# Kernel optimization log

Measured on AMD Instinct MI355X. Metric: run time of the kernel, lower is better.

The kernel has to match this reference:

```python
import jax, jax.numpy as jnp
import numpy as np

N_NODES = 100000
N_EDGES = 1600000
IN_C, HID_C, OUT_C = 128, 128, 64


def setup_inputs() -> dict:
    key = jax.random.key(0)
    k = jax.random.split(key, 5)
    x = jax.random.normal(k[0], (N_NODES, IN_C), dtype=jnp.float32)
    edge_index = jax.random.randint(k[1], (2, N_EDGES), 0, N_NODES, dtype=jnp.int32)
    # Glorot-ish scaling for the GCNConv linear weights
    W1 = jax.random.normal(k[2], (IN_C, HID_C), dtype=jnp.float32) * (1.0 / np.sqrt(IN_C))
    b1 = jnp.zeros((HID_C,), dtype=jnp.float32)
    W2 = jax.random.normal(k[3], (HID_C, OUT_C), dtype=jnp.float32) * (1.0 / np.sqrt(HID_C))
    b2 = jnp.zeros((OUT_C,), dtype=jnp.float32)
    return {"x": x, "edge_index": edge_index, "W1": W1, "b1": b1, "W2": W2, "b2": b2}


def _gcn_conv(h, W, b, src, dst, deg_inv_sqrt, n):
    # h: [N, F_in] -> linear transform, then deg-normalized scatter-add over edges
    h = h @ W  # [N, F_out]
    norm = deg_inv_sqrt[src] * deg_inv_sqrt[dst]  # [E+N] (self-loops included)
    msgs = h[src] * norm[:, None]  # gather + scale
    out = jax.ops.segment_sum(msgs, dst, num_segments=n)  # scatter-add to dst
    return out + b


def reference(x, edge_index, W1, b1, W2, b2):
    n = x.shape[0]
    loops = jnp.arange(n, dtype=edge_index.dtype)
    src = jnp.concatenate([edge_index[0], loops])  # add self-loops (PyG default)
    dst = jnp.concatenate([edge_index[1], loops])
    deg = jax.ops.segment_sum(jnp.ones_like(dst, dtype=x.dtype), dst, num_segments=n)
    deg_inv_sqrt = jax.lax.rsqrt(deg)  # deg >= 1 due to self-loops

    h = _gcn_conv(x, W1, b1, src, dst, deg_inv_sqrt, n)
    h = jax.nn.relu(h)
    # F.dropout(training=False) is identity at inference
    h = _gcn_conv(h, W2, b2, src, dst, deg_inv_sqrt, n)
    return jax.nn.log_softmax(h, axis=1)
```

## Files before the change

### kernel.cpp

```cpp
#include <hip/hip_runtime.h>
#include <hip/hip_bf16.h>


typedef unsigned short ushortT;
typedef unsigned char ucharT;
typedef __attribute__((ext_vector_type(8))) short short8v;
typedef __attribute__((ext_vector_type(4))) float float4v;
typedef __attribute__((ext_vector_type(2))) float float2v;
typedef __attribute__((ext_vector_type(8))) unsigned short ushort8v;

__device__ __forceinline__ float bf2f(ushortT u) {
  union { unsigned int i; float f; } x;
  x.i = ((unsigned int)u) << 16;
  return x.f;
}

__device__ __forceinline__ ushortT f2bf(float f) {
  __hip_bfloat16 h = __float2bfloat16(f);
  return *(ushortT*)&h;
}

__device__ __forceinline__ ucharT f2fp8(float f) {
  unsigned int w = __builtin_amdgcn_cvt_pk_fp8_f32(f, f, 0, false);
  return (ucharT)(w & 0xff);
}

__device__ __forceinline__ void fp8x8_to_f32(unsigned int lo, unsigned int hi,
                                             float* f) {
  float2v p0 = __builtin_amdgcn_cvt_pk_f32_fp8(lo, false);
  float2v p1 = __builtin_amdgcn_cvt_pk_f32_fp8(lo, true);
  float2v p2 = __builtin_amdgcn_cvt_pk_f32_fp8(hi, false);
  float2v p3 = __builtin_amdgcn_cvt_pk_f32_fp8(hi, true);
  f[0] = p0[0]; f[1] = p0[1]; f[2] = p1[0]; f[3] = p1[1];
  f[4] = p2[0]; f[5] = p2[1]; f[6] = p3[0]; f[7] = p3[1];
}

__device__ __forceinline__ void fp8x4_to_f32(unsigned int w, float* f) {
  float2v p0 = __builtin_amdgcn_cvt_pk_f32_fp8(w, false);
  float2v p1 = __builtin_amdgcn_cvt_pk_f32_fp8(w, true);
  f[0] = p0[0]; f[1] = p0[1]; f[2] = p1[0]; f[3] = p1[1];
}

__global__ void probe_k(const ushortT* __restrict__ xr, int* __restrict__ flag) {
  const int lane = threadIdx.x;
  float v = bf2f(xr[lane]);
  bool sane = isfinite(v) && fabsf(v) < 1e4f;
  unsigned long long m = __ballot(sane);
  if (lane == 0) flag[0] = (m == ~0ull) ? 1 : 0;
}

__global__ __launch_bounds__(256) void wprep_k(const void* __restrict__ W1v,
                                               const void* __restrict__ W2v,
                                               const int* __restrict__ flag,
                                               ushortT* __restrict__ Wt1,
                                               ushortT* __restrict__ Wt2) {
  const int i = blockIdx.x * 256 + threadIdx.x;
  const bool isbf = (flag[0] != 0);
  if (i < 16384) {
    int nn = i & 127, k = i >> 7;
    ushortT v = isbf ? ((const ushortT*)W1v)[k * 128 + nn]
                     : f2bf(((const float*)W1v)[k * 128 + nn]);
    Wt1[nn * 128 + k] = v;
  } else if (i < 24576) {
    int j = i - 16384;
    int nn = j & 63, k = j >> 6;
    ushortT v = isbf ? ((const ushortT*)W2v)[k * 64 + nn]
                     : f2bf(((const float*)W2v)[k * 64 + nn]);
    Wt2[nn * 128 + k] = v;
  }
}


__global__ __launch_bounds__(256) void bhist_k(const int* __restrict__ dst, int E, int B,
                                               int* __restrict__ gbc) {
  __shared__ int h[512];
  const int tid = threadIdx.x;
  for (int i = tid; i < B; i += 256) h[i] = 0;
  __syncthreads();
  const int i0 = blockIdx.x * 8192;
  const int iend = min(i0 + 8192, E);
  for (int i = i0 + tid; i < iend; i += 256) atomicAdd(&h[dst[i] >> 8], 1);
  __syncthreads();
  for (int i = tid; i < B; i += 256)
    if (h[i]) atomicAdd(&gbc[i], h[i]);
}

__global__ __launch_bounds__(256) void bscan_k(const int* __restrict__ gbc, int B,
                                               int* __restrict__ bbase,
                                               int* __restrict__ gcur) {
  __shared__ int p[256];
  const int t = threadIdx.x;
  int a = (2 * t < B) ? gbc[2 * t] : 0;
  int b = (2 * t + 1 < B) ? gbc[2 * t + 1] : 0;
  const int sum = a + b;
  p[t] = sum;
  __syncthreads();
  int run = sum;
  for (int off = 1; off < 256; off <<= 1) {
    int v = (t >= off) ? p[t - off] : 0;
    __syncthreads();
    run += v;
    p[t] = run;
    __syncthreads();
  }
  const int excl = run - sum;
  if (2 * t < B) { bbase[2 * t] = excl; gcur[2 * t] = excl; }
  if (2 * t + 1 < B) { bbase[2 * t + 1] = excl + a; gcur[2 * t + 1] = excl + a; }
}

__global__ __launch_bounds__(256) void bin_k(const int* __restrict__ srcv,
                                             const int* __restrict__ dstv, int E, int B,
                                             int* __restrict__ gcur,
                                             int* __restrict__ tmp) {
  __shared__ int hist[512];
  __shared__ int base[512];
  const int tid = threadIdx.x;
  const int i0 = blockIdx.x * 8192;
  const int iend = min(i0 + 8192, E);
  for (int i = tid; i < B; i += 256) hist[i] = 0;
  __syncthreads();
  for (int i = i0 + tid; i < iend; i += 256) atomicAdd(&hist[dstv[i] >> 8], 1);
  __syncthreads();
  for (int i = tid; i < B; i += 256) {
    int h = hist[i];
    base[i] = h ? atomicAdd(&gcur[i], h) : 0;
    hist[i] = 0;
  }
  __syncthreads();
  for (int i = i0 + tid; i < iend; i += 256) {
    int d = dstv[i];
    int s = srcv[i];
    int b = d >> 8;
    int l = atomicAdd(&hist[b], 1);
    tmp[base[b] + l] = s | ((d & 255) << 17);
  }
}

__global__ __launch_bounds__(256) void csr_k(const int* __restrict__ tmp,
                                             const int* __restrict__ bbase,
                                             const int* __restrict__ gbc, int n,
                                             int* __restrict__ row_ptr,
                                             int* __restrict__ cnt,
                                             float* __restrict__ dis,
                                             int* __restrict__ col) {
  __shared__ int lhist[256];
  __shared__ int lexcl[256];
  const int b = blockIdx.x;
  const int tid = threadIdx.x;
  const int e0 = bbase[b];
  const int e1 = e0 + gbc[b];
  lhist[tid] = 0;
  __syncthreads();
  for (int i = e0 + tid; i < e1; i += 256) atomicAdd(&lhist[tmp[i] >> 17], 1);
  __syncthreads();
  const int v = lhist[tid];
  int run = v;
  lexcl[tid] = run;
  __syncthreads();
  for (int off = 1; off < 256; off <<= 1) {
    int t = (tid >= off) ? lexcl[tid - off] : 0;
    __syncthreads();
    run += t;
    lexcl[tid] = run;
    __syncthreads();
  }
  const int excl = run - v;
  const int node = (b << 8) + tid;
  if (node < n) {
    row_ptr[node] = e0 + excl;
    cnt[node] = v;
    dis[node] = rsqrtf((float)(v + 1));
  }
  lhist[tid] = 0;
  lexcl[tid] = excl;
  __syncthreads();
  for (int i = e0 + tid; i < e1; i += 256) {
    int p = tmp[i];
    int dloc = p >> 17;
    int s = p & 131071;
    int l = atomicAdd(&lhist[dloc], 1);
    col[e0 + lexcl[dloc] + l] = s;
  }
}

__global__ __launch_bounds__(256) void gemm1_k(const void* __restrict__ xv,
                                               const ushortT* __restrict__ Wt1,
                                               const float* __restrict__ dis,
                                               const int* __restrict__ flag,
                                               ucharT* __restrict__ Hb8, int n) {
  __shared__ ushortT sA[64 * 132];
  __shared__ ushortT sW[128 * 132];
  const bool isbf = (flag[0] != 0);
  const int tid = threadIdx.x;
  const int rb = blockIdx.x * 64;
  const int wave = tid >> 6;
  const int lane = tid & 63;
  const int m = lane & 15;
  const int quad = lane >> 4;

  if (isbf) {
    for (int i = tid; i < 2048; i += 256) {
      int r = i >> 5, c4 = (i & 31) * 4;
      ushort4 u = make_ushort4(0, 0, 0, 0);
      if (rb + r < n) u = *(const ushort4*)((const ushortT*)xv + (size_t)(rb + r) * 128 + c4);
      *(ushort4*)&sA[r * 132 + c4] = u;
    }
  } else {
    for (int i = tid; i < 2048; i += 256) {
      int r = i >> 5, c4 = (i & 31) * 4;
      float4 v = make_float4(0.f, 0.f, 0.f, 0.f);
      if (rb + r < n) v = *(const float4*)((const float*)xv + (size_t)(rb + r) * 128 + c4);
      ushort4 u;
      u.x = f2bf(v.x); u.y = f2bf(v.y); u.z = f2bf(v.z); u.w = f2bf(v.w);
      *(ushort4*)&sA[r * 132 + c4] = u;
    }
  }
  for (int i = tid; i < 4096; i += 256) {
    int nn = i >> 5, k4 = (i & 31) * 4;
    *(ushort4*)&sW[nn * 132 + k4] = *(const ushort4*)&Wt1[nn * 128 + k4];
  }
  __syncthreads();

  float4v acc[8];
#pragma unroll
  for (int t = 0; t < 8; ++t) acc[t] = (float4v)(0.f);

  const int arow = wave * 16 + m;
#pragma unroll
  for (int kc = 0; kc < 4; ++kc) {
    short8v af = *(const short8v*)&sA[arow * 132 + kc * 32 + quad * 8];
#pragma unroll
    for (int nb = 0; nb < 8; ++nb) {
      short8v bf = *(const short8v*)&sW[(nb * 16 + m) * 132 + kc * 32 + quad * 8];
      acc[nb] = __builtin_amdgcn_mfma_f32_16x16x32_bf16(af, bf, acc[nb], 0, 0, 0);
    }
  }

#pragma unroll
  for (int r = 0; r < 4; ++r) {
    int grow = rb + wave * 16 + quad * 4 + r;
    if (grow <= n) {
      float sc = (grow < n) ? dis[grow] : 0.f;
#pragma unroll
      for (int nb = 0; nb < 8; ++nb)
        Hb8[(size_t)grow * 128 + nb * 16 + m] =
            (grow < n) ? f2fp8(sc * acc[nb][r]) : (ucharT)0;
    }
  }
}

__global__ __launch_bounds__(256) void agg1_k(const ucharT* __restrict__ Hb8,
                                              const int* __restrict__ col,
                                              const int* __restrict__ row_ptr,
                                              const int* __restrict__ count,
                                              const float* __restrict__ dis,
                                              const void* __restrict__ b1v,
                                              const int* __restrict__ flag,
                                              ushortT* __restrict__ Ab, int n) {
  const int node = blockIdx.x * 4 + (threadIdx.x >> 6);
  if (node >= n) return;
  const bool isbf = (flag[0] != 0);
  const int lane = threadIdx.x & 63;
  const int quad = lane >> 4;
  const int c8 = (lane & 15) * 8;
  const int start = __builtin_amdgcn_readfirstlane(row_ptr[node]);
  const int cnt = __builtin_amdgcn_readfirstlane(count[node]);

  float2v acc[4];
#pragma unroll
  for (int k = 0; k < 4; ++k) acc[k] = (float2v)(0.f);

  for (int e0 = 0; e0 < cnt; e0 += 16) {
#pragma unroll
    for (int g = 0; g < 4; ++g) {
      const int e = e0 + g * 4 + quad;
      int s = col[start + e];
      s = (e < cnt) ? s : n;
      uint2 h = *(const uint2*)&Hb8[((unsigned)s << 7) + (unsigned)c8];
      acc[0] += __builtin_amdgcn_cvt_pk_f32_fp8(h.x, false);
      acc[1] += __builtin_amdgcn_cvt_pk_f32_fp8(h.x, true);
      acc[2] += __builtin_amdgcn_cvt_pk_f32_fp8(h.y, false);
      acc[3] += __builtin_amdgcn_cvt_pk_f32_fp8(h.y, true);
    }
  }

  float accs[8];
#pragma unroll
  for (int k = 0; k < 4; ++k) { accs[2 * k] = acc[k][0]; accs[2 * k + 1] = acc[k][1]; }
#pragma unroll
  for (int k = 0; k < 8; ++k) {
    accs[k] += __shfl_xor(accs[k], 16);
    accs[k] += __shfl_xor(accs[k], 32);
  }

  const float din = dis[node];
  uint2 hsp = *(const uint2*)&Hb8[((unsigned)node << 7) + (unsigned)c8];
  float hs[8];
  fp8x8_to_f32(hsp.x, hsp.y, hs);
  float b[8];
  if (isbf) {
    ushort8v bb = *(const ushort8v*)((const ushortT*)b1v + c8);
#pragma unroll
    for (int k = 0; k < 8; ++k) b[k] = bf2f(bb[k]);
  } else {
    const float* bf = (const float*)b1v + c8;
#pragma unroll
    for (int k = 0; k < 8; ++k) b[k] = bf[k];
  }
  if (quad == 0) {
    ushort8v o;
#pragma unroll
    for (int k = 0; k < 8; ++k)
      o[k] = f2bf(fmaxf(fmaf(din, accs[k] + hs[k], b[k]), 0.f));
    *(ushort8v*)&Ab[(size_t)node * 128 + c8] = o;
  }
}

__global__ __launch_bounds__(256) void gemm2_k(const ushortT* __restrict__ Ab,
                                               const ushortT* __restrict__ Wt2,
                                               const float* __restrict__ dis,
                                               ucharT* __restrict__ H2b8, int n) {
  __shared__ ushortT sA[64 * 132];
  __shared__ ushortT sW[64 * 132];
  const int tid = threadIdx.x;
  const int rb = blockIdx.x * 64;
  const int wave = tid >> 6;
  const int lane = tid & 63;
  const int m = lane & 15;
  const int quad = lane >> 4;

  for (int i = tid; i < 2048; i += 256) {
    int r = i >> 5, c4 = (i & 31) * 4;
    ushort4 u = make_ushort4(0, 0, 0, 0);
    if (rb + r < n) u = *(const ushort4*)&Ab[(size_t)(rb + r) * 128 + c4];
    *(ushort4*)&sA[r * 132 + c4] = u;
  }
  for (int i = tid; i < 2048; i += 256) {
    int nn = i >> 5, k4 = (i & 31) * 4;
    *(ushort4*)&sW[nn * 132 + k4] = *(const ushort4*)&Wt2[nn * 128 + k4];
  }
  __syncthreads();

  float4v acc[4];
#pragma unroll
  for (int t = 0; t < 4; ++t) acc[t] = (float4v)(0.f);

  const int arow = wave * 16 + m;
#pragma unroll
  for (int kc = 0; kc < 4; ++kc) {
    short8v af = *(const short8v*)&sA[arow * 132 + kc * 32 + quad * 8];
#pragma unroll
    for (int nb = 0; nb < 4; ++nb) {
      short8v bf = *(const short8v*)&sW[(nb * 16 + m) * 132 + kc * 32 + quad * 8];
      acc[nb] = __builtin_amdgcn_mfma_f32_16x16x32_bf16(af, bf, acc[nb], 0, 0, 0);
    }
  }

#pragma unroll
  for (int r = 0; r < 4; ++r) {
    int grow = rb + wave * 16 + quad * 4 + r;
    if (grow <= n) {
      float sc = (grow < n) ? dis[grow] : 0.f;
#pragma unroll
      for (int nb = 0; nb < 4; ++nb)
        H2b8[(size_t)grow * 64 + nb * 16 + m] =
            (grow < n) ? f2fp8(sc * acc[nb][r]) : (ucharT)0;
    }
  }
}

__global__ __launch_bounds__(256) void agg2_k(const ucharT* __restrict__ H2b8,
                                              const int* __restrict__ col,
                                              const int* __restrict__ row_ptr,
                                              const int* __restrict__ count,
                                              const float* __restrict__ dis,
                                              const void* __restrict__ b2v,
                                              const int* __restrict__ flag,
                                              void* __restrict__ outv, int n) {
  const int node = blockIdx.x * 4 + (threadIdx.x >> 6);
  if (node >= n) return;
  const bool isbf = (flag[0] != 0);
  const int lane = threadIdx.x & 63;
  const int quad = lane >> 4;
  const int c4 = (lane & 15) * 4;
  const int start = __builtin_amdgcn_readfirstlane(row_ptr[node]);
  const int cnt = __builtin_amdgcn_readfirstlane(count[node]);

  float2v acc[2];
  acc[0] = (float2v)(0.f);
  acc[1] = (float2v)(0.f);

  for (int e0 = 0; e0 < cnt; e0 += 16) {
#pragma unroll
    for (int g = 0; g < 4; ++g) {
      const int e = e0 + g * 4 + quad;
      int s = col[start + e];
      s = (e < cnt) ? s : n;
      unsigned int h = *(const unsigned int*)&H2b8[((unsigned)s << 6) + (unsigned)c4];
      acc[0] += __builtin_amdgcn_cvt_pk_f32_fp8(h, false);
      acc[1] += __builtin_amdgcn_cvt_pk_f32_fp8(h, true);
    }
  }

  float av[4] = {acc[0][0], acc[0][1], acc[1][0], acc[1][1]};
#pragma unroll
  for (int k = 0; k < 4; ++k) {
    av[k] += __shfl_xor(av[k], 16);
    av[k] += __shfl_xor(av[k], 32);
  }

  const float din = dis[node];
  unsigned int hsp = *(const unsigned int*)&H2b8[((unsigned)node << 6) + (unsigned)c4];
  float hs[4];
  fp8x4_to_f32(hsp, hs);
  float b[4];
  if (isbf) {
    ushort4 bb = *(const ushort4*)((const ushortT*)b2v + c4);
    b[0] = bf2f(bb.x); b[1] = bf2f(bb.y); b[2] = bf2f(bb.z); b[3] = bf2f(bb.w);
  } else {
    const float* bf = (const float*)b2v + c4;
#pragma unroll
    for (int k = 0; k < 4; ++k) b[k] = bf[k];
  }
  float v[4];
#pragma unroll
  for (int k = 0; k < 4; ++k) v[k] = fmaf(din, av[k] + hs[k], b[k]);

  float mx = fmaxf(fmaxf(v[0], v[1]), fmaxf(v[2], v[3]));
  for (int off = 1; off < 16; off <<= 1) mx = fmaxf(mx, __shfl_xor(mx, off));
  float ssum = __expf(v[0] - mx) + __expf(v[1] - mx) + __expf(v[2] - mx) + __expf(v[3] - mx);
  for (int off = 1; off < 16; off <<= 1) ssum += __shfl_xor(ssum, off);
  const float lse = mx + __logf(ssum);

  if (quad == 0) {
    if (isbf) {
      ushort4 o;
      o.x = f2bf(v[0] - lse); o.y = f2bf(v[1] - lse);
      o.z = f2bf(v[2] - lse); o.w = f2bf(v[3] - lse);
      *(ushort4*)((__hip_bfloat16*)outv + (size_t)node * 64 + c4) = o;
    } else {
      float4 o = make_float4(v[0] - lse, v[1] - lse, v[2] - lse, v[3] - lse);
      *(float4*)((float*)outv + (size_t)node * 64 + c4) = o;
    }
  }
}


extern "C" void kernel_launch(void* const* d_in, const int* in_sizes, int n_in,
                              void* d_out, int out_size, void* d_ws, size_t ws_size,
                              hipStream_t stream) {
  const void* x  = d_in[0];
  const int*  ei = (const int*)d_in[1];
  const void* W1 = d_in[2];
  const void* b1 = d_in[3];
  const void* W2 = d_in[4];
  const void* b2 = d_in[5];

  const int n = in_sizes[0] / 128;
  const int E = in_sizes[1] / 2;
  const int B = (n + 255) >> 8;
  const int* srcv = ei;
  const int* dstv = ei + E;

  char* p = (char*)d_ws;
  auto alloc = [&](size_t bytes) {
    char* q = p;
    p += (bytes + 255) & ~(size_t)255;
    return q;
  };
  ucharT* Hb8 = (ucharT*)alloc((size_t)(n + 1) * 128);
  ucharT* H2b8 = (ucharT*)alloc((size_t)(n + 1) * 64);
  ushortT* Ab = (ushortT*)alloc((size_t)n * 128 * 2);
  float* dis = (float*)alloc((size_t)n * 4);
  int* cntA = (int*)alloc((size_t)n * 4);
  int* row_ptr = (int*)alloc((size_t)n * 4);
  int* gbc = (int*)alloc(512 * 4);
  int* bbase = (int*)alloc(512 * 4);
  int* gcur = (int*)alloc(512 * 4);
  int* flag = (int*)alloc(64 * 4);
  ushortT* Wt1 = (ushortT*)alloc(16384 * 2);
  ushortT* Wt2 = (ushortT*)alloc(8192 * 2);
  int* tmp = (int*)alloc((size_t)E * 4);
  int* col = (int*)alloc(((size_t)E + 64) * 4);

  (void)hipMemsetAsync(gbc, 0, 512 * sizeof(int), stream);

  const int gChunks = (E + 8191) / 8192;

  probe_k<<<1, 64, 0, stream>>>((const ushortT*)x, flag);
  wprep_k<<<96, 256, 0, stream>>>(W1, W2, flag, Wt1, Wt2);
  bhist_k<<<gChunks, 256, 0, stream>>>(dstv, E, B, gbc);
  bscan_k<<<1, 256, 0, stream>>>(gbc, B, bbase, gcur);
  bin_k<<<gChunks, 256, 0, stream>>>(srcv, dstv, E, B, gcur, tmp);
  csr_k<<<B, 256, 0, stream>>>(tmp, bbase, gbc, n, row_ptr, cntA, dis, col);

  gemm1_k<<<(n + 63) / 64, 256, 0, stream>>>(x, Wt1, dis, flag, Hb8, n);
  agg1_k<<<(n + 3) / 4, 256, 0, stream>>>(Hb8, col, row_ptr, cntA, dis, b1, flag, Ab, n);
  gemm2_k<<<(n + 63) / 64, 256, 0, stream>>>(Ab, Wt2, dis, H2b8, n);
  agg2_k<<<(n + 3) / 4, 256, 0, stream>>>(H2b8, col, row_ptr, cntA, dis, b2, flag, d_out, n);
}
```

Before: 282.6 us.

## Map four nodes per wave in aggregation, pack row_ptr/count, inline dtype probe

The aggregation kernels now give each 16-lane quarter-wave its own destination node instead of spreading one node's edges across the whole wave. This removes the cross-quad shuffle reduction and the idle lanes on low-degree nodes, but the loop runs to the maximum degree among the four nodes, so lanes diverge when degrees differ. Row pointer and count are packed into one int2 so each node needs a single load. The separate probe kernel is dropped and every kernel recomputes the dtype check with a ballot, which saves one launch. The col buffer padding is enlarged to cover the longer over-reads.

Result: faster. 256.8 us (-9.1%).

```diff
diff --git a/kernel.cpp b/kernel.cpp
--- a/kernel.cpp
+++ b/kernel.cpp
@@ -41,21 +41,21 @@
   f[0] = p0[0]; f[1] = p0[1]; f[2] = p1[0]; f[3] = p1[1];
 }
 
-__global__ void probe_k(const ushortT* __restrict__ xr, int* __restrict__ flag) {
-  const int lane = threadIdx.x;
+__device__ __forceinline__ bool probe_isbf(const void* xv) {
+  const ushortT* xr = (const ushortT*)xv;
+  const int lane = threadIdx.x & 63;
   float v = bf2f(xr[lane]);
   bool sane = isfinite(v) && fabsf(v) < 1e4f;
-  unsigned long long m = __ballot(sane);
-  if (lane == 0) flag[0] = (m == ~0ull) ? 1 : 0;
+  return __ballot(sane) == ~0ull;
 }
 
 __global__ __launch_bounds__(256) void wprep_k(const void* __restrict__ W1v,
                                                const void* __restrict__ W2v,
-                                               const int* __restrict__ flag,
+                                               const void* __restrict__ xv,
                                                ushortT* __restrict__ Wt1,
                                                ushortT* __restrict__ Wt2) {
+  const bool isbf = probe_isbf(xv);
   const int i = blockIdx.x * 256 + threadIdx.x;
-  const bool isbf = (flag[0] != 0);
   if (i < 16384) {
     int nn = i & 127, k = i >> 7;
     ushortT v = isbf ? ((const ushortT*)W1v)[k * 128 + nn]
@@ -139,8 +139,7 @@
 __global__ __launch_bounds__(256) void csr_k(const int* __restrict__ tmp,
                                              const int* __restrict__ bbase,
                                              const int* __restrict__ gbc, int n,
-                                             int* __restrict__ row_ptr,
-                                             int* __restrict__ cnt,
+                                             int2* __restrict__ rpc,
                                              float* __restrict__ dis,
                                              int* __restrict__ col) {
   __shared__ int lhist[256];
@@ -167,8 +166,7 @@
   const int excl = run - v;
   const int node = (b << 8) + tid;
   if (node < n) {
-    row_ptr[node] = e0 + excl;
-    cnt[node] = v;
+    rpc[node] = make_int2(e0 + excl, v);
     dis[node] = rsqrtf((float)(v + 1));
   }
   lhist[tid] = 0;
@@ -186,11 +184,10 @@
 __global__ __launch_bounds__(256) void gemm1_k(const void* __restrict__ xv,
                                                const ushortT* __restrict__ Wt1,
                                                const float* __restrict__ dis,
-                                               const int* __restrict__ flag,
                                                ucharT* __restrict__ Hb8, int n) {
   __shared__ ushortT sA[64 * 132];
   __shared__ ushortT sW[128 * 132];
-  const bool isbf = (flag[0] != 0);
+  const bool isbf = probe_isbf(xv);
   const int tid = threadIdx.x;
   const int rb = blockIdx.x * 64;
   const int wave = tid >> 6;
@@ -251,32 +248,55 @@
 
 __global__ __launch_bounds__(256) void agg1_k(const ucharT* __restrict__ Hb8,
                                               const int* __restrict__ col,
-                                              const int* __restrict__ row_ptr,
-                                              const int* __restrict__ count,
+                                              const int2* __restrict__ rpc,
                                               const float* __restrict__ dis,
                                               const void* __restrict__ b1v,
-                                              const int* __restrict__ flag,
+                                              const void* __restrict__ xv,
                                               ushortT* __restrict__ Ab, int n) {
-  const int node = blockIdx.x * 4 + (threadIdx.x >> 6);
-  if (node >= n) return;
-  const bool isbf = (flag[0] != 0);
-  const int lane = threadIdx.x & 63;
+  const bool isbf = probe_isbf(xv);
+  const int tid = threadIdx.x;
+  const int lane = tid & 63;
+  const int wave = tid >> 6;
   const int quad = lane >> 4;
-  const int c8 = (lane & 15) * 8;
-  const int start = __builtin_amdgcn_readfirstlane(row_ptr[node]);
-  const int cnt = __builtin_amdgcn_readfirstlane(count[node]);
+  const int m = lane & 15;
+  const int c8 = m * 8;
+  const int node = blockIdx.x * 16 + wave * 4 + quad;
+  const bool valid = node < n;
+  const int nd = valid ? node : (n - 1);
+
+  const int2 rc = rpc[nd];
+  const int start = rc.x;
+  const int cnt = valid ? rc.y : 0;
+  const float din = dis[nd];
+
+  const uint2 hsp = *(const uint2*)&Hb8[((unsigned)(valid ? node : n) << 7) + (unsigned)c8];
+  float b[8];
+  if (isbf) {
+    ushort8v bb = *(const ushort8v*)((const ushortT*)b1v + c8);
+#pragma unroll
+    for (int k = 0; k < 8; ++k) b[k] = bf2f(bb[k]);
+  } else {
+    const float* bf = (const float*)b1v + c8;
+#pragma unroll
+    for (int k = 0; k < 8; ++k) b[k] = bf[k];
+  }
+
+  int cmax = cnt;
+  cmax = max(cmax, __shfl_xor(cmax, 16));
+  cmax = max(cmax, __shfl_xor(cmax, 32));
+  const int cmaxs = __builtin_amdgcn_readfirstlane(cmax);
 
   float2v acc[4];
 #pragma unroll
   for (int k = 0; k < 4; ++k) acc[k] = (float2v)(0.f);
 
-  for (int e0 = 0; e0 < cnt; e0 += 16) {
-#pragma unroll
-    for (int g = 0; g < 4; ++g) {
-      const int e = e0 + g * 4 + quad;
-      int s = col[start + e];
-      s = (e < cnt) ? s : n;
-      uint2 h = *(const uint2*)&Hb8[((unsigned)s << 7) + (unsigned)c8];
+  for (int e = 0; e < cmaxs; e += 4) {
+#pragma unroll
+    for (int u = 0; u < 4; ++u) {
+      const int ee = e + u;
+      int s = col[start + ee];
+      s = (ee < cnt) ? s : n;
+      const uint2 h = *(const uint2*)&Hb8[((unsigned)s << 7) + (unsigned)c8];
       acc[0] += __builtin_amdgcn_cvt_pk_f32_fp8(h.x, false);
       acc[1] += __builtin_amdgcn_cvt_pk_f32_fp8(h.x, true);
       acc[2] += __builtin_amdgcn_cvt_pk_f32_fp8(h.y, false);
@@ -284,34 +304,15 @@
     }
   }
 
-  float accs[8];
-#pragma unroll
-  for (int k = 0; k < 4; ++k) { accs[2 * k] = acc[k][0]; accs[2 * k + 1] = acc[k][1]; }
-#pragma unroll
-  for (int k = 0; k < 8; ++k) {
-    accs[k] += __shfl_xor(accs[k], 16);
-    accs[k] += __shfl_xor(accs[k], 32);
-  }
-
-  const float din = dis[node];
-  uint2 hsp = *(const uint2*)&Hb8[((unsigned)node << 7) + (unsigned)c8];
-  float hs[8];
-  fp8x8_to_f32(hsp.x, hsp.y, hs);
-  float b[8];
-  if (isbf) {
-    ushort8v bb = *(const ushort8v*)((const ushortT*)b1v + c8);
-#pragma unroll
-    for (int k = 0; k < 8; ++k) b[k] = bf2f(bb[k]);
-  } else {
-    const float* bf = (const float*)b1v + c8;
-#pragma unroll
-    for (int k = 0; k < 8; ++k) b[k] = bf[k];
-  }
-  if (quad == 0) {
+  if (valid) {
+    float hs[8];
+    fp8x8_to_f32(hsp.x, hsp.y, hs);
     ushort8v o;
 #pragma unroll
-    for (int k = 0; k < 8; ++k)
-      o[k] = f2bf(fmaxf(fmaf(din, accs[k] + hs[k], b[k]), 0.f));
+    for (int k = 0; k < 4; ++k) {
+      o[2 * k]     = f2bf(fmaxf(fmaf(din, acc[k][0] + hs[2 * k],     b[2 * k]),     0.f));
+      o[2 * k + 1] = f2bf(fmaxf(fmaf(din, acc[k][1] + hs[2 * k + 1], b[2 * k + 1]), 0.f));
+    }
     *(ushort8v*)&Ab[(size_t)node * 128 + c8] = o;
   }
 }
@@ -371,48 +372,29 @@
 
 __global__ __launch_bounds__(256) void agg2_k(const ucharT* __restrict__ H2b8,
                                               const int* __restrict__ col,
-                                              const int* __restrict__ row_ptr,
-                                              const int* __restrict__ count,
+                                              const int2* __restrict__ rpc,
                                               const float* __restrict__ dis,
                                               const void* __restrict__ b2v,
-                                              const int* __restrict__ flag,
+                                              const void* __restrict__ xv,
                                               void* __restrict__ outv, int n) {
-  const int node = blockIdx.x * 4 + (threadIdx.x >> 6);
-  if (node >= n) return;
-  const bool isbf = (flag[0] != 0);
-  const int lane = threadIdx.x & 63;
+  const bool isbf = probe_isbf(xv);
+  const int tid = threadIdx.x;
+  const int lane = tid & 63;
+  const int wave = tid >> 6;
   const int quad = lane >> 4;
-  const int c4 = (lane & 15) * 4;
-  const int start = __builtin_amdgcn_readfirstlane(row_ptr[node]);
-  const int cnt = __builtin_amdgcn_readfirstlane(count[node]);
-
-  float2v acc[2];
-  acc[0] = (float2v)(0.f);
-  acc[1] = (float2v)(0.f);
-
-  for (int e0 = 0; e0 < cnt; e0 += 16) {
-#pragma unroll
-    for (int g = 0; g < 4; ++g) {
-      const int e = e0 + g * 4 + quad;
-      int s = col[start + e];
-      s = (e < cnt) ? s : n;
-      unsigned int h = *(const unsigned int*)&H2b8[((unsigned)s << 6) + (unsigned)c4];
-      acc[0] += __builtin_amdgcn_cvt_pk_f32_fp8(h, false);
-      acc[1] += __builtin_amdgcn_cvt_pk_f32_fp8(h, true);
-    }
-  }
-
-  float av[4] = {acc[0][0], acc[0][1], acc[1][0], acc[1][1]};
-#pragma unroll
-  for (int k = 0; k < 4; ++k) {
-    av[k] += __shfl_xor(av[k], 16);
-    av[k] += __shfl_xor(av[k], 32);
-  }
-
-  const float din = dis[node];
-  unsigned int hsp = *(const unsigned int*)&H2b8[((unsigned)node << 6) + (unsigned)c4];
-  float hs[4];
-  fp8x4_to_f32(hsp, hs);
+  const int m = lane & 15;
+  const int c4 = m * 4;
+  const int node = blockIdx.x * 16 + wave * 4 + quad;
+  const bool valid = node < n;
+  const int nd = valid ? node : (n - 1);
+
+  const int2 rc = rpc[nd];
+  const int start = rc.x;
+  const int cnt = valid ? rc.y : 0;
+  const float din = dis[nd];
+
+  const unsigned int hsp =
+      *(const unsigned int*)&H2b8[((unsigned)(valid ? node : n) << 6) + (unsigned)c4];
   float b[4];
   if (isbf) {
     ushort4 bb = *(const ushort4*)((const ushortT*)b2v + c4);
@@ -422,9 +404,35 @@
 #pragma unroll
     for (int k = 0; k < 4; ++k) b[k] = bf[k];
   }
+
+  int cmax = cnt;
+  cmax = max(cmax, __shfl_xor(cmax, 16));
+  cmax = max(cmax, __shfl_xor(cmax, 32));
+  const int cmaxs = __builtin_amdgcn_readfirstlane(cmax);
+
+  float2v acc[2];
+  acc[0] = (float2v)(0.f);
+  acc[1] = (float2v)(0.f);
+
+  for (int e = 0; e < cmaxs; e += 4) {
+#pragma unroll
+    for (int u = 0; u < 4; ++u) {
+      const int ee = e + u;
+      int s = col[start + ee];
+      s = (ee < cnt) ? s : n;
+      const unsigned int h = *(const unsigned int*)&H2b8[((unsigned)s << 6) + (unsigned)c4];
+      acc[0] += __builtin_amdgcn_cvt_pk_f32_fp8(h, false);
+      acc[1] += __builtin_amdgcn_cvt_pk_f32_fp8(h, true);
+    }
+  }
+
+  float hs[4];
+  fp8x4_to_f32(hsp, hs);
   float v[4];
-#pragma unroll
-  for (int k = 0; k < 4; ++k) v[k] = fmaf(din, av[k] + hs[k], b[k]);
+  v[0] = fmaf(din, acc[0][0] + hs[0], b[0]);
+  v[1] = fmaf(din, acc[0][1] + hs[1], b[1]);
+  v[2] = fmaf(din, acc[1][0] + hs[2], b[2]);
+  v[3] = fmaf(din, acc[1][1] + hs[3], b[3]);
 
   float mx = fmaxf(fmaxf(v[0], v[1]), fmaxf(v[2], v[3]));
   for (int off = 1; off < 16; off <<= 1) mx = fmaxf(mx, __shfl_xor(mx, off));
@@ -432,7 +440,7 @@
   for (int off = 1; off < 16; off <<= 1) ssum += __shfl_xor(ssum, off);
   const float lse = mx + __logf(ssum);
 
-  if (quad == 0) {
+  if (valid) {
     if (isbf) {
       ushort4 o;
       o.x = f2bf(v[0] - lse); o.y = f2bf(v[1] - lse);
@@ -472,30 +480,27 @@
   ucharT* H2b8 = (ucharT*)alloc((size_t)(n + 1) * 64);
   ushortT* Ab = (ushortT*)alloc((size_t)n * 128 * 2);
   float* dis = (float*)alloc((size_t)n * 4);
-  int* cntA = (int*)alloc((size_t)n * 4);
-  int* row_ptr = (int*)alloc((size_t)n * 4);
+  int2* rpc = (int2*)alloc((size_t)n * 8);
   int* gbc = (int*)alloc(512 * 4);
   int* bbase = (int*)alloc(512 * 4);
   int* gcur = (int*)alloc(512 * 4);
-  int* flag = (int*)alloc(64 * 4);
   ushortT* Wt1 = (ushortT*)alloc(16384 * 2);
   ushortT* Wt2 = (ushortT*)alloc(8192 * 2);
   int* tmp = (int*)alloc((size_t)E * 4);
-  int* col = (int*)alloc(((size_t)E + 64) * 4);
+  int* col = (int*)alloc(((size_t)E + 4096) * 4);
 
   (void)hipMemsetAsync(gbc, 0, 512 * sizeof(int), stream);
 
   const int gChunks = (E + 8191) / 8192;
 
-  probe_k<<<1, 64, 0, stream>>>((const ushortT*)x, flag);
-  wprep_k<<<96, 256, 0, stream>>>(W1, W2, flag, Wt1, Wt2);
+  wprep_k<<<96, 256, 0, stream>>>(W1, W2, x, Wt1, Wt2);
   bhist_k<<<gChunks, 256, 0, stream>>>(dstv, E, B, gbc);
   bscan_k<<<1, 256, 0, stream>>>(gbc, B, bbase, gcur);
   bin_k<<<gChunks, 256, 0, stream>>>(srcv, dstv, E, B, gcur, tmp);
-  csr_k<<<B, 256, 0, stream>>>(tmp, bbase, gbc, n, row_ptr, cntA, dis, col);
-
-  gemm1_k<<<(n + 63) / 64, 256, 0, stream>>>(x, Wt1, dis, flag, Hb8, n);
-  agg1_k<<<(n + 3) / 4, 256, 0, stream>>>(Hb8, col, row_ptr, cntA, dis, b1, flag, Ab, n);
+  csr_k<<<B, 256, 0, stream>>>(tmp, bbase, gbc, n, rpc, dis, col);
+
+  gemm1_k<<<(n + 63) / 64, 256, 0, stream>>>(x, Wt1, dis, Hb8, n);
+  agg1_k<<<(n + 15) / 16, 256, 0, stream>>>(Hb8, col, rpc, dis, b1, x, Ab, n);
   gemm2_k<<<(n + 63) / 64, 256, 0, stream>>>(Ab, Wt2, dis, H2b8, n);
-  agg2_k<<<(n + 3) / 4, 256, 0, stream>>>(H2b8, col, row_ptr, cntA, dis, b2, flag, d_out, n);
-}
+  agg2_k<<<(n + 15) / 16, 256, 0, stream>>>(H2b8, col, rpc, dis, b2, x, d_out, n);
+}
```
